# Kernel tuning notes

Hardware: AMD Instinct MI355X
Metric: run time of the kernel (lower is better)

Reference implementation:

```python
import jax, jax.numpy as jnp
import numpy as np

N, E, D_IN, HID, H, L = 20000, 320000, 64, 128, 4, 3
D_HEAD = HID  # PyG TransformerConv: out_channels is the per-head dim
LN_EPS = 1e-5


def setup_inputs() -> dict:
    key = jax.random.key(0)
    ks = jax.random.split(key, 12)
    x = jax.random.normal(ks[0], (N, D_IN), dtype=jnp.float32)
    edge_index = jax.random.randint(ks[1], (2, E), 0, N, dtype=jnp.int64)
    s_in = 1.0 / np.sqrt(D_IN)
    s_h = 1.0 / np.sqrt(HID)
    Win = jax.random.normal(ks[2], (D_IN, HID), dtype=jnp.float32) * s_in
    bin_ = jnp.zeros((HID,), dtype=jnp.float32)
    Wq = jax.random.normal(ks[3], (L, HID, H * D_HEAD), dtype=jnp.float32) * s_h
    Wk = jax.random.normal(ks[4], (L, HID, H * D_HEAD), dtype=jnp.float32) * s_h
    Wv = jax.random.normal(ks[5], (L, HID, H * D_HEAD), dtype=jnp.float32) * s_h
    bq = jnp.zeros((L, H * D_HEAD), dtype=jnp.float32)
    bk = jnp.zeros((L, H * D_HEAD), dtype=jnp.float32)
    bv = jnp.zeros((L, H * D_HEAD), dtype=jnp.float32)
    Wskip = jax.random.normal(ks[6], (L, HID, HID), dtype=jnp.float32) * s_h
    bskip = jnp.zeros((L, HID), dtype=jnp.float32)
    ln_gamma = jnp.ones((L, HID), dtype=jnp.float32)
    ln_beta = jnp.zeros((L, HID), dtype=jnp.float32)
    return dict(x=x, edge_index=edge_index, Win=Win, bin_=bin_, Wq=Wq, bq=bq,
                Wk=Wk, bk=bk, Wv=Wv, bv=bv, Wskip=Wskip, bskip=bskip,
                ln_gamma=ln_gamma, ln_beta=ln_beta)


def _segment_softmax(logits, seg, num_segments):
    # logits: [E, H], seg: [E] destination node ids
    m = jax.ops.segment_max(logits, seg, num_segments=num_segments)  # [N, H]
    ex = jnp.exp(logits - m[seg])
    s = jax.ops.segment_sum(ex, seg, num_segments=num_segments)  # [N, H]
    return ex / (s[seg] + 1e-16)


def _layer_norm(x, gamma, beta):
    mu = jnp.mean(x, axis=-1, keepdims=True)
    var = jnp.mean(jnp.square(x - mu), axis=-1, keepdims=True)
    return (x - mu) * jax.lax.rsqrt(var + LN_EPS) * gamma + beta


def _transformer_conv(h, src, dst, Wq, bq, Wk, bk, Wv, bv, Wskip, bskip):
    q = (h @ Wq + bq).reshape(N, H, D_HEAD)
    k = (h @ Wk + bk).reshape(N, H, D_HEAD)
    v = (h @ Wv + bv).reshape(N, H, D_HEAD)
    scale = 1.0 / np.sqrt(D_HEAD)
    logits = jnp.einsum('ehd,ehd->eh', q[dst], k[src]) * scale  # [E, H]
    alpha = _segment_softmax(logits, dst, N)  # [E, H]
    msg = alpha[:, :, None] * v[src]  # [E, H, D_HEAD]
    out = jax.ops.segment_sum(msg, dst, num_segments=N)  # [N, H, D_HEAD]
    out = out.mean(axis=1)  # concat=False -> mean over heads
    return out + h @ Wskip + bskip  # root_weight skip (lin_skip)


def reference(x, edge_index, Win, bin_, Wq, bq, Wk, bk, Wv, bv, Wskip, bskip, ln_gamma, ln_beta):
    src = edge_index[0]
    dst = edge_index[1]
    h = x @ Win + bin_
    for l in range(L):
        h_new = _transformer_conv(h, src, dst, Wq[l], bq[l], Wk[l], bk[l],
                                  Wv[l], bv[l], Wskip[l], bskip[l])
        h = _layer_norm(h + h_new, ln_gamma[l], ln_beta[l])
    return h
```

## Files before the change

### kernel.cpp

```cpp
#include <hip/hip_runtime.h>
#include <hip/hip_bf16.h>
#include <math.h>

#define NN 20000
#define EE 320000
#define DIN 64
#define HIDC 128
#define NCOLS 1664
#define NL 3

typedef __attribute__((ext_vector_type(8))) short bf16x8;
typedef __attribute__((ext_vector_type(8))) unsigned short u16x8;
typedef __attribute__((ext_vector_type(4))) float f32x4;

__device__ __forceinline__ float bf2f(unsigned short u) {
  union { unsigned i; float f; } v; v.i = ((unsigned)u) << 16; return v.f;
}
__device__ __forceinline__ unsigned short f2bf(float f) {
  __hip_bfloat16 b = __float2bfloat16(f);
  return *(unsigned short*)&b;
}

__device__ __forceinline__ unsigned char f2fp8(float f) {
#if __has_builtin(__builtin_amdgcn_cvt_pk_fp8_f32)
  return (unsigned char)(__builtin_amdgcn_cvt_pk_fp8_f32(f, f, 0, 0) & 0xFF);
#else
  unsigned b = __float_as_uint(f);
  unsigned s = (b >> 24) & 0x80u;
  float a = fabsf(f);
  if (a < 0.015625f) return (unsigned char)s;
  unsigned mag = __float_as_uint(fminf(a, 448.f));
  mag += 0x7FFFFu + ((mag >> 20) & 1u);
  unsigned code = (mag >> 20) - (120u << 3);
  if (code > 0x7Eu) code = 0x7Eu;
  return (unsigned char)(s | code);
#endif
}

__device__ __forceinline__ float fp82f(unsigned b) {
  unsigned x = ((b & 0x80u) << 24) | ((b & 0x7fu) << 20);
  return __uint_as_float(x) * 0x1p+120f;
}

__device__ __forceinline__ void dec8(uint2 u, float* f) {
#if __has_builtin(__builtin_amdgcn_cvt_pk_f32_fp8)
  {
    auto p0 = __builtin_amdgcn_cvt_pk_f32_fp8(u.x, 0);
    auto p1 = __builtin_amdgcn_cvt_pk_f32_fp8(u.x, 1);
    auto p2 = __builtin_amdgcn_cvt_pk_f32_fp8(u.y, 0);
    auto p3 = __builtin_amdgcn_cvt_pk_f32_fp8(u.y, 1);
    f[0] = p0[0]; f[1] = p0[1]; f[2] = p1[0]; f[3] = p1[1];
    f[4] = p2[0]; f[5] = p2[1]; f[6] = p3[0]; f[7] = p3[1];
  }
#else
#pragma unroll
  for (int i = 0; i < 4; i++) f[i] = fp82f((u.x >> (8 * i)) & 0xFFu);
#pragma unroll
  for (int i = 0; i < 4; i++) f[4 + i] = fp82f((u.y >> (8 * i)) & 0xFFu);
#endif
}

__global__ void build_wcatT(const float* __restrict__ Wq, const float* __restrict__ Wk,
                            const float* __restrict__ Wv, const float* __restrict__ Wsk,
                            unsigned short* __restrict__ wT) {
  int idx = blockIdx.x * 256 + threadIdx.x;
  if (idx >= NCOLS * HIDC) return;
  int n = idx >> 7, k = idx & 127;
  float v;
  if (n < 512)       v = Wq[(size_t)k * 512 + n];
  else if (n < 1024) v = Wk[(size_t)k * 512 + (n - 512)];
  else if (n < 1536) v = Wv[(size_t)k * 512 + (n - 1024)];
  else               v = Wsk[(size_t)k * 128 + (n - 1536)];
  wT[idx] = f2bf(v);
}

__global__ void build_winT(const float* __restrict__ Win, unsigned short* __restrict__ winT) {
  int idx = blockIdx.x * 256 + threadIdx.x;
  if (idx >= HIDC * DIN) return;
  int c = idx >> 6, k = idx & 63;
  winT[idx] = f2bf(Win[(size_t)k * HIDC + c]);
}

__global__ void build_bcat(const float* __restrict__ bq, const float* __restrict__ bk,
                           const float* __restrict__ bv, const float* __restrict__ bsk,
                           float* __restrict__ bcat) {
  int m = blockIdx.x * 256 + threadIdx.x;
  if (m >= NCOLS) return;
  float v;
  if (m < 512)       v = bq[m];
  else if (m < 1024) v = bk[m - 512];
  else if (m < 1536) v = bv[m - 1024];
  else               v = bsk[m - 1536];
  bcat[m] = v;
}

__global__ void conv_x(const float* __restrict__ x, unsigned short* __restrict__ xb) {
  int i = blockIdx.x * 256 + threadIdx.x;
  if (i * 4 >= NN * DIN) return;
  float4 v = *(const float4*)(x + (size_t)i * 4);
  ushort4 o = make_ushort4(f2bf(v.x), f2bf(v.y), f2bf(v.z), f2bf(v.w));
  *(ushort4*)(xb + (size_t)i * 4) = o;
}

__global__ void deg_hist(const int* __restrict__ ei, int* __restrict__ deg) {
  int e = blockIdx.x * 256 + threadIdx.x;
  if (e >= EE) return;
  atomicAdd(&deg[ei[EE + e]], 1);
}

__global__ __launch_bounds__(1024) void scan_deg(const int* __restrict__ deg,
                                                 int* __restrict__ rowstart) {
  __shared__ int part[1024];
  int t = threadIdx.x;
  int base = t * 20;
  int local[20];
  int s = 0;
#pragma unroll
  for (int i = 0; i < 20; i++) {
    int idx = base + i;
    int d = (idx < NN) ? deg[idx] : 0;
    local[i] = d;
    s += d;
  }
  part[t] = s;
  __syncthreads();
  for (int d = 1; d < 1024; d <<= 1) {
    int v = (t >= d) ? part[t - d] : 0;
    __syncthreads();
    part[t] += v;
    __syncthreads();
  }
  int run = part[t] - s;
#pragma unroll
  for (int i = 0; i < 20; i++) {
    int idx = base + i;
    if (idx < NN) rowstart[idx] = run;
    run += local[i];
  }
  if (t == 1023) rowstart[NN] = part[1023];
}

__global__ void csr_scatter(const int* __restrict__ ei, const int* __restrict__ rowstart,
                            int* __restrict__ cur, int* __restrict__ csrc) {
  int e = blockIdx.x * 256 + threadIdx.x;
  if (e >= EE) return;
  int src = ei[e], dst = ei[EE + e];
  int pos = atomicAdd(&cur[dst], 1);
  csrc[rowstart[dst] + pos] = src;
}

__device__ __forceinline__ void gl_lds16(const void* g, void* l) {
  __builtin_amdgcn_global_load_lds((const unsigned int*)g, (unsigned int*)l, 16, 0, 0);
}

template <int K>
__device__ __forceinline__ void stage_tile(const unsigned short* gbase,
                                           unsigned char* lbase, int tid) {
  constexpr int CH = K / 8;
  constexpr int ISS = (128 * CH) / 256;
  int wave = tid >> 6;
#pragma unroll
  for (int p = 0; p < ISS; p++) {
    int slot = p * 256 + tid;
    int row = slot / CH, ch = slot % CH;
    const unsigned short* src = gbase + (size_t)row * K + ((ch ^ (row & 7)) * 8);
    unsigned char* ldst = lbase + (size_t)(p * 256 + wave * 64) * 16;
    gl_lds16(src, ldst);
  }
}

template <int K>
__device__ __forceinline__ bf16x8 read_frag(const unsigned char* lbase, int row, int kk, int lk) {
  int ch = (kk * 4 + lk) ^ (row & 7);
  return *(const bf16x8*)(lbase + (size_t)row * (K * 2) + ch * 16);
}

template <int K, int MODE>
__global__ __launch_bounds__(256) void mfma_gemm_t(
    const unsigned short* __restrict__ A, const unsigned short* __restrict__ BT,
    const float* __restrict__ bias, unsigned short* __restrict__ outb,
    unsigned char* __restrict__ outkv, float* __restrict__ outf,
    int nbx, int nwg) {
  constexpr int LDSZ = (512 * K > 34816) ? 512 * K : 34816;
  __shared__ __align__(16) unsigned char LDS[LDSZ];
  const int tid = threadIdx.x;

  int orig = blockIdx.x;
  int q = nwg >> 3, r = nwg & 7;
  int xcd = orig & 7, slot = orig >> 3;
  int wg = (xcd < r ? xcd * (q + 1) : r * (q + 1) + (xcd - r) * q) + slot;
  const int bx = wg % nbx, by = wg / nbx;

  const int lane = tid & 63;
  const int wave = tid >> 6;
  const int lm = lane & 15, lk = lane >> 4;
  const int wm = wave >> 1, wn = wave & 1;
  const int row0 = by * 128, col0 = bx * 128;
  unsigned char* aL = LDS;
  unsigned char* bL = LDS + 128 * K * 2;

  stage_tile<K>(A + (size_t)row0 * K, aL, tid);
  stage_tile<K>(BT + (size_t)col0 * K, bL, tid);
  __syncthreads();

  constexpr int KK = K / 32;
  f32x4 acc[4][4] = {};
  bf16x8 af[4][KK];
#pragma unroll
  for (int mf = 0; mf < 4; mf++)
#pragma unroll
    for (int kk = 0; kk < KK; kk++)
      af[mf][kk] = read_frag<K>(aL, wm * 64 + mf * 16 + lm, kk, lk);

#pragma unroll
  for (int nf = 0; nf < 4; nf++) {
    bf16x8 bf[KK];
#pragma unroll
    for (int kk = 0; kk < KK; kk++)
      bf[kk] = read_frag<K>(bL, wn * 64 + nf * 16 + lm, kk, lk);
#pragma unroll
    for (int mf = 0; mf < 4; mf++)
#pragma unroll
      for (int kk = 0; kk < KK; kk++)
        acc[mf][nf] = __builtin_amdgcn_mfma_f32_16x16x32_bf16(af[mf][kk], bf[kk],
                                                              acc[mf][nf], 0, 0, 0);
  }
  __syncthreads();

  if (MODE == 0 && bx == 12) {
#pragma unroll
    for (int nf = 0; nf < 4; nf++) {
      int c = wn * 64 + nf * 16 + lm;
      float bv = bias[col0 + c];
#pragma unroll
      for (int mf = 0; mf < 4; mf++)
#pragma unroll
        for (int i = 0; i < 4; i++) {
          int rr = row0 + wm * 64 + mf * 16 + lk * 4 + i;
          if (rr < NN) outf[(size_t)rr * HIDC + c] = acc[mf][nf][i] + bv;
        }
    }
  } else if (MODE == 0 && bx >= 4) {
    unsigned char* bb8 = LDS;
#pragma unroll
    for (int nf = 0; nf < 4; nf++) {
      int c = wn * 64 + nf * 16 + lm;
      float bv = bias[col0 + c];
#pragma unroll
      for (int mf = 0; mf < 4; mf++)
#pragma unroll
        for (int i = 0; i < 4; i++) {
          int row = wm * 64 + mf * 16 + lk * 4 + i;
          bb8[row * 144 + c] = f2fp8(acc[mf][nf][i] + bv);
        }
    }
    __syncthreads();
    const int kvcol0 = col0 - 512;
#pragma unroll
    for (int p = 0; p < 4; p++) {
      int idx = p * 256 + tid;
      int row = idx >> 3, cw = idx & 7;
      int gr = row0 + row;
      if (gr < NN) {
        uint4 v = *(const uint4*)(bb8 + row * 144 + cw * 16);
        *(uint4*)(outkv + (size_t)gr * 1024 + kvcol0 + cw * 16) = v;
      }
    }
  } else {
    unsigned short* bb = (unsigned short*)LDS;
#pragma unroll
    for (int nf = 0; nf < 4; nf++) {
      int c = wn * 64 + nf * 16 + lm;
      float bv = bias[col0 + c];
#pragma unroll
      for (int mf = 0; mf < 4; mf++)
#pragma unroll
        for (int i = 0; i < 4; i++) {
          int row = wm * 64 + mf * 16 + lk * 4 + i;
          bb[row * 136 + c] = f2bf(acc[mf][nf][i] + bv);
          if (MODE == 1) {
            int rr = row0 + row;
            if (rr < NN) outf[(size_t)rr * HIDC + c] = acc[mf][nf][i] + bv;
          }
        }
    }
    __syncthreads();
    constexpr int STRIDE = (MODE == 0) ? 512 : HIDC;
#pragma unroll
    for (int p = 0; p < 8; p++) {
      int idx = p * 256 + tid;
      int row = idx >> 4, c = idx & 15;
      int gr = row0 + row;
      if (gr < NN) {
        uint4 v = *(const uint4*)(bb + row * 136 + c * 8);
        *(uint4*)(outb + (size_t)gr * STRIDE + col0 + c * 8) = v;
      }
    }
  }
}

__global__ __launch_bounds__(256) void node_fused(
    const unsigned short* __restrict__ qb, const unsigned char* __restrict__ kv8,
    const float* __restrict__ skipb,
    const float* __restrict__ h, const int* __restrict__ rowstart,
    const int* __restrict__ csrc,
    const float* __restrict__ gamma, const float* __restrict__ beta,
    float* __restrict__ outp, unsigned short* __restrict__ hb_out) {
  int n = blockIdx.x * 4 + (threadIdx.x >> 6);
  if (n >= NN) return;
  int lane = threadIdx.x & 63;
  int hh = lane >> 4, t = lane & 15;
  int j0 = rowstart[n], j1 = rowstart[n + 1];

  u16x8 q8 = *(const u16x8*)(qb + (size_t)n * 512 + hh * 128 + t * 8);
  float qf[8];
#pragma unroll
  for (int i = 0; i < 8; i++) qf[i] = bf2f(q8[i]);

  const unsigned char* kb = kv8 + hh * 128 + t * 8;
  const unsigned char* vb = kv8 + 512 + hh * 128 + t * 8;

  float m = -INFINITY, s = 0.f;
  float acc[8] = {0.f, 0.f, 0.f, 0.f, 0.f, 0.f, 0.f, 0.f};

  int j = j0;
  for (; j + 1 < j1; j += 2) {
    int sA = csrc[j], sB = csrc[j + 1];
    uint2 kA = *(const uint2*)(kb + (size_t)sA * 1024);
    uint2 vA = *(const uint2*)(vb + (size_t)sA * 1024);
    uint2 kB = *(const uint2*)(kb + (size_t)sB * 1024);
    uint2 vB = *(const uint2*)(vb + (size_t)sB * 1024);
    float kfA[8], kfB[8];
    dec8(kA, kfA); dec8(kB, kfB);
    float pA = 0.f, pB = 0.f;
#pragma unroll
    for (int i = 0; i < 8; i++) { pA += qf[i] * kfA[i]; pB += qf[i] * kfB[i]; }
    pA += __shfl_xor(pA, 1); pB += __shfl_xor(pB, 1);
    pA += __shfl_xor(pA, 2); pB += __shfl_xor(pB, 2);
    pA += __shfl_xor(pA, 4); pB += __shfl_xor(pB, 4);
    pA += __shfl_xor(pA, 8); pB += __shfl_xor(pB, 8);
    float lgA = pA * 0.08838834764831845f;
    float lgB = pB * 0.08838834764831845f;
    float vfA[8], vfB[8];
    dec8(vA, vfA); dec8(vB, vfB);
    if (lgA > m) {
      float r = __expf(m - lgA);
      s *= r;
#pragma unroll
      for (int i = 0; i < 8; i++) acc[i] *= r;
      m = lgA;
    }
    float wA = __expf(lgA - m);
    s += wA;
#pragma unroll
    for (int i = 0; i < 8; i++) acc[i] += wA * vfA[i];
    if (lgB > m) {
      float r = __expf(m - lgB);
      s *= r;
#pragma unroll
      for (int i = 0; i < 8; i++) acc[i] *= r;
      m = lgB;
    }
    float wB = __expf(lgB - m);
    s += wB;
#pragma unroll
    for (int i = 0; i < 8; i++) acc[i] += wB * vfB[i];
  }
  if (j < j1) {
    int sA = csrc[j];
    uint2 kA = *(const uint2*)(kb + (size_t)sA * 1024);
    uint2 vA = *(const uint2*)(vb + (size_t)sA * 1024);
    float kfA[8], vfA[8];
    dec8(kA, kfA); dec8(vA, vfA);
    float pA = 0.f;
#pragma unroll
    for (int i = 0; i < 8; i++) pA += qf[i] * kfA[i];
    pA += __shfl_xor(pA, 1);
    pA += __shfl_xor(pA, 2);
    pA += __shfl_xor(pA, 4);
    pA += __shfl_xor(pA, 8);
    float lgA = pA * 0.08838834764831845f;
    if (lgA > m) {
      float r = __expf(m - lgA);
      s *= r;
#pragma unroll
      for (int i = 0; i < 8; i++) acc[i] *= r;
      m = lgA;
    }
    float wA = __expf(lgA - m);
    s += wA;
#pragma unroll
    for (int i = 0; i < 8; i++) acc[i] += wA * vfA[i];
  }

  float rsel = 0.25f / (s + 1e-16f);
#pragma unroll
  for (int i = 0; i < 8; i++) {
    float a = acc[i] * rsel;
    a += __shfl_xor(a, 16);
    a += __shfl_xor(a, 32);
    acc[i] = a;
  }

  size_t hbase = (size_t)n * HIDC;
  float u[8];
  {
    float4 h0 = *(const float4*)(h + hbase + t * 8);
    float4 h1 = *(const float4*)(h + hbase + t * 8 + 4);
    float4 k0 = *(const float4*)(skipb + hbase + t * 8);
    float4 k1 = *(const float4*)(skipb + hbase + t * 8 + 4);
    u[0] = h0.x + acc[0] + k0.x; u[1] = h0.y + acc[1] + k0.y;
    u[2] = h0.z + acc[2] + k0.z; u[3] = h0.w + acc[3] + k0.w;
    u[4] = h1.x + acc[4] + k1.x; u[5] = h1.y + acc[5] + k1.y;
    u[6] = h1.z + acc[6] + k1.z; u[7] = h1.w + acc[7] + k1.w;
  }
  float su = 0.f;
#pragma unroll
  for (int i = 0; i < 8; i++) su += u[i];
#pragma unroll
  for (int d = 1; d < 16; d <<= 1) su += __shfl_xor(su, d);
  float mu = su * (1.f / 128.f);
  float vs = 0.f;
#pragma unroll
  for (int i = 0; i < 8; i++) { u[i] -= mu; vs += u[i] * u[i]; }
#pragma unroll
  for (int d = 1; d < 16; d <<= 1) vs += __shfl_xor(vs, d);
  float inv = rsqrtf(vs * (1.f / 128.f) + 1e-5f);
  if (hh == 0) {
    float4 g0 = *(const float4*)(gamma + t * 8);
    float4 g1 = *(const float4*)(gamma + t * 8 + 4);
    float4 b0 = *(const float4*)(beta + t * 8);
    float4 b1 = *(const float4*)(beta + t * 8 + 4);
    float o[8];
    o[0] = u[0] * inv * g0.x + b0.x; o[1] = u[1] * inv * g0.y + b0.y;
    o[2] = u[2] * inv * g0.z + b0.z; o[3] = u[3] * inv * g0.w + b0.w;
    o[4] = u[4] * inv * g1.x + b1.x; o[5] = u[5] * inv * g1.y + b1.y;
    o[6] = u[6] * inv * g1.z + b1.z; o[7] = u[7] * inv * g1.w + b1.w;
    *(float4*)(outp + hbase + t * 8)     = make_float4(o[0], o[1], o[2], o[3]);
    *(float4*)(outp + hbase + t * 8 + 4) = make_float4(o[4], o[5], o[6], o[7]);
    ushort4 c0 = make_ushort4(f2bf(o[0]), f2bf(o[1]), f2bf(o[2]), f2bf(o[3]));
    ushort4 c1 = make_ushort4(f2bf(o[4]), f2bf(o[5]), f2bf(o[6]), f2bf(o[7]));
    *(ushort4*)(hb_out + hbase + t * 8)     = c0;
    *(ushort4*)(hb_out + hbase + t * 8 + 4) = c1;
  }
}

#define OFF_H      ((size_t)0)
#define OFF_SKIP   ((size_t)2560000)
#define OFF_QB     ((size_t)5120000)
#define OFF_KV8    ((size_t)10240000)
#define OFF_HB     ((size_t)15360000)
#define OFF_XB     ((size_t)16640000)
#define OFF_WT     ((size_t)17280000)
#define OFF_WINT   ((size_t)17386496)
#define OFF_BCAT   ((size_t)17390592)
#define OFF_CSRC   ((size_t)17392256)
#define OFF_ROW    ((size_t)17712256)
#define OFF_DEG    ((size_t)17732260)
#define OFF_CUR    ((size_t)17752260)

extern "C" void kernel_launch(void* const* d_in, const int* in_sizes, int n_in,
                              void* d_out, int out_size, void* d_ws, size_t ws_size,
                              hipStream_t stream) {
  const float* x    = (const float*)d_in[0];
  const int*   ei   = (const int*)d_in[1];
  const float* Win  = (const float*)d_in[2];
  const float* bin_ = (const float*)d_in[3];
  const float* Wq   = (const float*)d_in[4];
  const float* bq   = (const float*)d_in[5];
  const float* Wk   = (const float*)d_in[6];
  const float* bk   = (const float*)d_in[7];
  const float* Wv   = (const float*)d_in[8];
  const float* bv   = (const float*)d_in[9];
  const float* Wsk  = (const float*)d_in[10];
  const float* bsk  = (const float*)d_in[11];
  const float* lng  = (const float*)d_in[12];
  const float* lnb  = (const float*)d_in[13];
  float* out = (float*)d_out;
  float* ws = (float*)d_ws;

  float* h     = ws + OFF_H;
  float* skipb = ws + OFF_SKIP;
  unsigned short* qb   = (unsigned short*)(ws + OFF_QB);
  unsigned char*  kv8  = (unsigned char*)(ws + OFF_KV8);
  unsigned short* hb   = (unsigned short*)(ws + OFF_HB);
  unsigned short* xb   = (unsigned short*)(ws + OFF_XB);
  unsigned short* wT   = (unsigned short*)(ws + OFF_WT);
  unsigned short* winT = (unsigned short*)(ws + OFF_WINT);
  float* bcat  = ws + OFF_BCAT;
  int* csrc     = (int*)(ws + OFF_CSRC);
  int* rowstart = (int*)(ws + OFF_ROW);
  int* deg      = (int*)(ws + OFF_DEG);
  int* cur      = (int*)(ws + OFF_CUR);

  hipMemsetAsync(deg, 0, NN * sizeof(int), stream);
  hipMemsetAsync(cur, 0, NN * sizeof(int), stream);
  deg_hist<<<(EE + 255) / 256, 256, 0, stream>>>(ei, deg);
  scan_deg<<<1, 1024, 0, stream>>>(deg, rowstart);
  csr_scatter<<<(EE + 255) / 256, 256, 0, stream>>>(ei, rowstart, cur, csrc);

  conv_x<<<(NN * DIN / 4 + 255) / 256, 256, 0, stream>>>(x, xb);
  build_winT<<<(HIDC * DIN + 255) / 256, 256, 0, stream>>>(Win, winT);
  {
    const int nby = (NN + 127) / 128;
    mfma_gemm_t<64, 1><<<nby, 256, 0, stream>>>(xb, winT, bin_, hb, kv8, h, 1, nby);
  }

  for (int l = 0; l < NL; ++l) {
    build_wcatT<<<(NCOLS * HIDC + 255) / 256, 256, 0, stream>>>(
        Wq + (size_t)l * HIDC * 512, Wk + (size_t)l * HIDC * 512,
        Wv + (size_t)l * HIDC * 512, Wsk + (size_t)l * HIDC * HIDC, wT);
    build_bcat<<<(NCOLS + 255) / 256, 256, 0, stream>>>(
        bq + (size_t)l * 512, bk + (size_t)l * 512, bv + (size_t)l * 512,
        bsk + (size_t)l * 128, bcat);

    {
      const int nbx = NCOLS / 128;
      const int nby = (NN + 127) / 128;
      const int nwg = nbx * nby;
      mfma_gemm_t<128, 0><<<nwg, 256, 0, stream>>>(hb, wT, bcat, qb, kv8, skipb,
                                                   nbx, nwg);
    }

    float* dst = (l == NL - 1) ? out : h;
    node_fused<<<(NN + 3) / 4, 256, 0, stream>>>(
        qb, kv8, skipb, h, rowstart, csrc,
        lng + (size_t)l * 128, lnb + (size_t)l * 128, dst, hb);
  }
  (void)in_sizes; (void)n_in; (void)out_size; (void)ws_size;
}
```

Baseline: 331.3 us.

## Shrink projection GEMM tiles to 64x64, batch weight prep, unroll edge loop by four

```diff
diff --git a/kernel.cpp b/kernel.cpp
--- a/kernel.cpp
+++ b/kernel.cpp
@@ -60,18 +60,34 @@
 #endif
 }
 
-__global__ void build_wcatT(const float* __restrict__ Wq, const float* __restrict__ Wk,
-                            const float* __restrict__ Wv, const float* __restrict__ Wsk,
-                            unsigned short* __restrict__ wT) {
+__global__ void build_wcatT_all(const float* __restrict__ Wq, const float* __restrict__ Wk,
+                                const float* __restrict__ Wv, const float* __restrict__ Wsk,
+                                unsigned short* __restrict__ wT) {
   int idx = blockIdx.x * 256 + threadIdx.x;
-  if (idx >= NCOLS * HIDC) return;
-  int n = idx >> 7, k = idx & 127;
+  if (idx >= NL * NCOLS * HIDC) return;
+  int l = idx / (NCOLS * HIDC);
+  int rem = idx - l * (NCOLS * HIDC);
+  int n = rem >> 7, k = rem & 127;
   float v;
-  if (n < 512)       v = Wq[(size_t)k * 512 + n];
-  else if (n < 1024) v = Wk[(size_t)k * 512 + (n - 512)];
-  else if (n < 1536) v = Wv[(size_t)k * 512 + (n - 1024)];
-  else               v = Wsk[(size_t)k * 128 + (n - 1536)];
+  if (n < 512)       v = Wq[(size_t)l * HIDC * 512 + (size_t)k * 512 + n];
+  else if (n < 1024) v = Wk[(size_t)l * HIDC * 512 + (size_t)k * 512 + (n - 512)];
+  else if (n < 1536) v = Wv[(size_t)l * HIDC * 512 + (size_t)k * 512 + (n - 1024)];
+  else               v = Wsk[(size_t)l * HIDC * HIDC + (size_t)k * 128 + (n - 1536)];
   wT[idx] = f2bf(v);
+}
+
+__global__ void build_bcat_all(const float* __restrict__ bq, const float* __restrict__ bk,
+                               const float* __restrict__ bv, const float* __restrict__ bsk,
+                               float* __restrict__ bcat) {
+  int idx = blockIdx.x * 256 + threadIdx.x;
+  if (idx >= NL * NCOLS) return;
+  int l = idx / NCOLS, m = idx - l * NCOLS;
+  float v;
+  if (m < 512)       v = bq[l * 512 + m];
+  else if (m < 1024) v = bk[l * 512 + (m - 512)];
+  else if (m < 1536) v = bv[l * 512 + (m - 1024)];
+  else               v = bsk[l * 128 + (m - 1536)];
+  bcat[idx] = v;
 }
 
 __global__ void build_winT(const float* __restrict__ Win, unsigned short* __restrict__ winT) {
@@ -79,19 +95,6 @@
   if (idx >= HIDC * DIN) return;
   int c = idx >> 6, k = idx & 63;
   winT[idx] = f2bf(Win[(size_t)k * HIDC + c]);
-}
-
-__global__ void build_bcat(const float* __restrict__ bq, const float* __restrict__ bk,
-                           const float* __restrict__ bv, const float* __restrict__ bsk,
-                           float* __restrict__ bcat) {
-  int m = blockIdx.x * 256 + threadIdx.x;
-  if (m >= NCOLS) return;
-  float v;
-  if (m < 512)       v = bq[m];
-  else if (m < 1024) v = bk[m - 512];
-  else if (m < 1536) v = bv[m - 1024];
-  else               v = bsk[m - 1536];
-  bcat[m] = v;
 }
 
 __global__ void conv_x(const float* __restrict__ x, unsigned short* __restrict__ xb) {
@@ -175,125 +178,197 @@
   return *(const bf16x8*)(lbase + (size_t)row * (K * 2) + ch * 16);
 }
 
-template <int K, int MODE>
-__global__ __launch_bounds__(256) void mfma_gemm_t(
+__global__ __launch_bounds__(256) void mfma_gemm_in(
     const unsigned short* __restrict__ A, const unsigned short* __restrict__ BT,
     const float* __restrict__ bias, unsigned short* __restrict__ outb,
-    unsigned char* __restrict__ outkv, float* __restrict__ outf,
-    int nbx, int nwg) {
-  constexpr int LDSZ = (512 * K > 34816) ? 512 * K : 34816;
-  __shared__ __align__(16) unsigned char LDS[LDSZ];
+    float* __restrict__ outf) {
+  __shared__ __align__(16) unsigned char LDS[34816];
   const int tid = threadIdx.x;
-
-  int orig = blockIdx.x;
-  int q = nwg >> 3, r = nwg & 7;
-  int xcd = orig & 7, slot = orig >> 3;
-  int wg = (xcd < r ? xcd * (q + 1) : r * (q + 1) + (xcd - r) * q) + slot;
-  const int bx = wg % nbx, by = wg / nbx;
-
-  const int lane = tid & 63;
-  const int wave = tid >> 6;
+  const int lane = tid & 63, wave = tid >> 6;
   const int lm = lane & 15, lk = lane >> 4;
   const int wm = wave >> 1, wn = wave & 1;
-  const int row0 = by * 128, col0 = bx * 128;
+  const int row0 = blockIdx.x * 128, col0 = 0;
   unsigned char* aL = LDS;
-  unsigned char* bL = LDS + 128 * K * 2;
-
-  stage_tile<K>(A + (size_t)row0 * K, aL, tid);
-  stage_tile<K>(BT + (size_t)col0 * K, bL, tid);
+  unsigned char* bL = LDS + 128 * 64 * 2;
+
+  stage_tile<64>(A + (size_t)row0 * 64, aL, tid);
+  stage_tile<64>(BT + (size_t)col0 * 64, bL, tid);
   __syncthreads();
 
-  constexpr int KK = K / 32;
   f32x4 acc[4][4] = {};
-  bf16x8 af[4][KK];
+  bf16x8 af[4][2];
 #pragma unroll
   for (int mf = 0; mf < 4; mf++)
 #pragma unroll
-    for (int kk = 0; kk < KK; kk++)
-      af[mf][kk] = read_frag<K>(aL, wm * 64 + mf * 16 + lm, kk, lk);
-
+    for (int kk = 0; kk < 2; kk++)
+      af[mf][kk] = read_frag<64>(aL, wm * 64 + mf * 16 + lm, kk, lk);
 #pragma unroll
   for (int nf = 0; nf < 4; nf++) {
-    bf16x8 bf[KK];
-#pragma unroll
-    for (int kk = 0; kk < KK; kk++)
-      bf[kk] = read_frag<K>(bL, wn * 64 + nf * 16 + lm, kk, lk);
+    bf16x8 bf[2];
+#pragma unroll
+    for (int kk = 0; kk < 2; kk++)
+      bf[kk] = read_frag<64>(bL, wn * 64 + nf * 16 + lm, kk, lk);
 #pragma unroll
     for (int mf = 0; mf < 4; mf++)
 #pragma unroll
-      for (int kk = 0; kk < KK; kk++)
+      for (int kk = 0; kk < 2; kk++)
         acc[mf][nf] = __builtin_amdgcn_mfma_f32_16x16x32_bf16(af[mf][kk], bf[kk],
                                                               acc[mf][nf], 0, 0, 0);
   }
   __syncthreads();
 
-  if (MODE == 0 && bx == 12) {
-#pragma unroll
-    for (int nf = 0; nf < 4; nf++) {
-      int c = wn * 64 + nf * 16 + lm;
+  unsigned short* bb = (unsigned short*)LDS;
+#pragma unroll
+  for (int nf = 0; nf < 4; nf++) {
+    int c = wn * 64 + nf * 16 + lm;
+    float bv = bias[c];
+#pragma unroll
+    for (int mf = 0; mf < 4; mf++)
+#pragma unroll
+      for (int i = 0; i < 4; i++) {
+        int row = wm * 64 + mf * 16 + lk * 4 + i;
+        float o = acc[mf][nf][i] + bv;
+        bb[row * 136 + c] = f2bf(o);
+        int r = row0 + row;
+        if (r < NN) outf[(size_t)r * HIDC + c] = o;
+      }
+  }
+  __syncthreads();
+#pragma unroll
+  for (int p = 0; p < 8; p++) {
+    int idx = p * 256 + tid;
+    int row = idx >> 4, c = idx & 15;
+    int gr = row0 + row;
+    if (gr < NN) {
+      uint4 v = *(const uint4*)(bb + row * 136 + c * 8);
+      *(uint4*)(outb + (size_t)gr * HIDC + c * 8) = v;
+    }
+  }
+}
+
+__global__ __launch_bounds__(256, 5) void gemm64(
+    const unsigned short* __restrict__ A, const unsigned short* __restrict__ BT,
+    const float* __restrict__ bias, unsigned short* __restrict__ qb,
+    unsigned char* __restrict__ kv8, float* __restrict__ skipb,
+    int nbx, int nwg) {
+  __shared__ __align__(16) unsigned char LDS[32768];
+  const int tid = threadIdx.x;
+  int orig = blockIdx.x;
+  int qq = nwg >> 3, rr8 = nwg & 7;
+  int xcd = orig & 7, slot = orig >> 3;
+  int wg = (xcd < rr8 ? xcd * (qq + 1) : rr8 * (qq + 1) + (xcd - rr8) * qq) + slot;
+  const int bx = wg % nbx, by = wg / nbx;
+
+  const int lane = tid & 63, wave = tid >> 6;
+  const int lm = lane & 15, lk = lane >> 4;
+  const int wm = wave >> 1, wn = wave & 1;
+  const int row0 = by * 64, col0 = bx * 64;
+  unsigned char* aL = LDS;
+  unsigned char* bL = LDS + 16384;
+
+  {
+    const unsigned short* gA = A + (size_t)row0 * 128;
+    const unsigned short* gB = BT + (size_t)col0 * 128;
+#pragma unroll
+    for (int p = 0; p < 4; p++) {
+      int sl = p * 256 + tid;
+      int row = sl >> 4, ch = sl & 15;
+      gl_lds16(gA + (size_t)row * 128 + ((ch ^ (row & 7)) * 8),
+               aL + (size_t)(p * 256 + wave * 64) * 16);
+    }
+#pragma unroll
+    for (int p = 0; p < 4; p++) {
+      int sl = p * 256 + tid;
+      int row = sl >> 4, ch = sl & 15;
+      gl_lds16(gB + (size_t)row * 128 + ((ch ^ (row & 7)) * 8),
+               bL + (size_t)(p * 256 + wave * 64) * 16);
+    }
+  }
+  __syncthreads();
+
+  f32x4 acc[2][2] = {};
+  bf16x8 af[2][4], bf[2][4];
+#pragma unroll
+  for (int mf = 0; mf < 2; mf++)
+#pragma unroll
+    for (int kk = 0; kk < 4; kk++)
+      af[mf][kk] = read_frag<128>(aL, wm * 32 + mf * 16 + lm, kk, lk);
+#pragma unroll
+  for (int nf = 0; nf < 2; nf++)
+#pragma unroll
+    for (int kk = 0; kk < 4; kk++)
+      bf[nf][kk] = read_frag<128>(bL, wn * 32 + nf * 16 + lm, kk, lk);
+#pragma unroll
+  for (int nf = 0; nf < 2; nf++)
+#pragma unroll
+    for (int mf = 0; mf < 2; mf++)
+#pragma unroll
+      for (int kk = 0; kk < 4; kk++)
+        acc[mf][nf] = __builtin_amdgcn_mfma_f32_16x16x32_bf16(af[mf][kk], bf[nf][kk],
+                                                              acc[mf][nf], 0, 0, 0);
+  __syncthreads();
+
+  if (bx >= 24) {
+    const int cbase = col0 - 1536;
+#pragma unroll
+    for (int nf = 0; nf < 2; nf++) {
+      int c = wn * 32 + nf * 16 + lm;
       float bv = bias[col0 + c];
 #pragma unroll
-      for (int mf = 0; mf < 4; mf++)
+      for (int mf = 0; mf < 2; mf++)
 #pragma unroll
         for (int i = 0; i < 4; i++) {
-          int rr = row0 + wm * 64 + mf * 16 + lk * 4 + i;
-          if (rr < NN) outf[(size_t)rr * HIDC + c] = acc[mf][nf][i] + bv;
+          int r = row0 + wm * 32 + mf * 16 + lk * 4 + i;
+          if (r < NN) skipb[(size_t)r * HIDC + cbase + c] = acc[mf][nf][i] + bv;
         }
     }
-  } else if (MODE == 0 && bx >= 4) {
+  } else if (bx >= 8) {
     unsigned char* bb8 = LDS;
 #pragma unroll
-    for (int nf = 0; nf < 4; nf++) {
-      int c = wn * 64 + nf * 16 + lm;
+    for (int nf = 0; nf < 2; nf++) {
+      int c = wn * 32 + nf * 16 + lm;
       float bv = bias[col0 + c];
 #pragma unroll
-      for (int mf = 0; mf < 4; mf++)
+      for (int mf = 0; mf < 2; mf++)
 #pragma unroll
         for (int i = 0; i < 4; i++) {
-          int row = wm * 64 + mf * 16 + lk * 4 + i;
-          bb8[row * 144 + c] = f2fp8(acc[mf][nf][i] + bv);
+          int row = wm * 32 + mf * 16 + lk * 4 + i;
+          bb8[row * 80 + c] = f2fp8(acc[mf][nf][i] + bv);
         }
     }
     __syncthreads();
     const int kvcol0 = col0 - 512;
-#pragma unroll
-    for (int p = 0; p < 4; p++) {
+    {
+      int row = tid >> 2, cw = tid & 3;
+      int gr = row0 + row;
+      if (gr < NN) {
+        uint4 v = *(const uint4*)(bb8 + row * 80 + cw * 16);
+        *(uint4*)(kv8 + (size_t)gr * 1024 + kvcol0 + cw * 16) = v;
+      }
+    }
+  } else {
+    unsigned short* bb = (unsigned short*)LDS;
+#pragma unroll
+    for (int nf = 0; nf < 2; nf++) {
+      int c = wn * 32 + nf * 16 + lm;
+      float bv = bias[col0 + c];
+#pragma unroll
+      for (int mf = 0; mf < 2; mf++)
+#pragma unroll
+        for (int i = 0; i < 4; i++) {
+          int row = wm * 32 + mf * 16 + lk * 4 + i;
+          bb[row * 80 + c] = f2bf(acc[mf][nf][i] + bv);
+        }
+    }
+    __syncthreads();
+#pragma unroll
+    for (int p = 0; p < 2; p++) {
       int idx = p * 256 + tid;
       int row = idx >> 3, cw = idx & 7;
       int gr = row0 + row;
       if (gr < NN) {
-        uint4 v = *(const uint4*)(bb8 + row * 144 + cw * 16);
-        *(uint4*)(outkv + (size_t)gr * 1024 + kvcol0 + cw * 16) = v;
-      }
-    }
-  } else {
-    unsigned short* bb = (unsigned short*)LDS;
-#pragma unroll
-    for (int nf = 0; nf < 4; nf++) {
-      int c = wn * 64 + nf * 16 + lm;
-      float bv = bias[col0 + c];
-#pragma unroll
-      for (int mf = 0; mf < 4; mf++)
-#pragma unroll
-        for (int i = 0; i < 4; i++) {
-          int row = wm * 64 + mf * 16 + lk * 4 + i;
-          bb[row * 136 + c] = f2bf(acc[mf][nf][i] + bv);
-          if (MODE == 1) {
-            int rr = row0 + row;
-            if (rr < NN) outf[(size_t)rr * HIDC + c] = acc[mf][nf][i] + bv;
-          }
-        }
-    }
-    __syncthreads();
-    constexpr int STRIDE = (MODE == 0) ? 512 : HIDC;
-#pragma unroll
-    for (int p = 0; p < 8; p++) {
-      int idx = p * 256 + tid;
-      int row = idx >> 4, c = idx & 15;
-      int gr = row0 + row;
-      if (gr < NN) {
-        uint4 v = *(const uint4*)(bb + row * 136 + c * 8);
-        *(uint4*)(outb + (size_t)gr * STRIDE + col0 + c * 8) = v;
+        uint4 v = *(const uint4*)(bb + row * 80 + cw * 8);
+        *(uint4*)(qb + (size_t)gr * 512 + col0 + cw * 8) = v;
       }
     }
   }
@@ -324,49 +399,49 @@
   float acc[8] = {0.f, 0.f, 0.f, 0.f, 0.f, 0.f, 0.f, 0.f};
 
   int j = j0;
-  for (; j + 1 < j1; j += 2) {
-    int sA = csrc[j], sB = csrc[j + 1];
-    uint2 kA = *(const uint2*)(kb + (size_t)sA * 1024);
-    uint2 vA = *(const uint2*)(vb + (size_t)sA * 1024);
-    uint2 kB = *(const uint2*)(kb + (size_t)sB * 1024);
-    uint2 vB = *(const uint2*)(vb + (size_t)sB * 1024);
-    float kfA[8], kfB[8];
-    dec8(kA, kfA); dec8(kB, kfB);
-    float pA = 0.f, pB = 0.f;
-#pragma unroll
-    for (int i = 0; i < 8; i++) { pA += qf[i] * kfA[i]; pB += qf[i] * kfB[i]; }
-    pA += __shfl_xor(pA, 1); pB += __shfl_xor(pB, 1);
-    pA += __shfl_xor(pA, 2); pB += __shfl_xor(pB, 2);
-    pA += __shfl_xor(pA, 4); pB += __shfl_xor(pB, 4);
-    pA += __shfl_xor(pA, 8); pB += __shfl_xor(pB, 8);
-    float lgA = pA * 0.08838834764831845f;
-    float lgB = pB * 0.08838834764831845f;
-    float vfA[8], vfB[8];
-    dec8(vA, vfA); dec8(vB, vfB);
-    if (lgA > m) {
-      float r = __expf(m - lgA);
-      s *= r;
-#pragma unroll
-      for (int i = 0; i < 8; i++) acc[i] *= r;
-      m = lgA;
-    }
-    float wA = __expf(lgA - m);
-    s += wA;
-#pragma unroll
-    for (int i = 0; i < 8; i++) acc[i] += wA * vfA[i];
-    if (lgB > m) {
-      float r = __expf(m - lgB);
-      s *= r;
-#pragma unroll
-      for (int i = 0; i < 8; i++) acc[i] *= r;
-      m = lgB;
-    }
-    float wB = __expf(lgB - m);
-    s += wB;
-#pragma unroll
-    for (int i = 0; i < 8; i++) acc[i] += wB * vfB[i];
-  }
-  if (j < j1) {
+  for (; j + 3 < j1; j += 4) {
+    int s4[4];
+#pragma unroll
+    for (int e = 0; e < 4; e++) s4[e] = csrc[j + e];
+    uint2 kk4[4], vv4[4];
+#pragma unroll
+    for (int e = 0; e < 4; e++) {
+      kk4[e] = *(const uint2*)(kb + (size_t)s4[e] * 1024);
+      vv4[e] = *(const uint2*)(vb + (size_t)s4[e] * 1024);
+    }
+    float lg4[4];
+#pragma unroll
+    for (int e = 0; e < 4; e++) {
+      float kf[8];
+      dec8(kk4[e], kf);
+      float p = 0.f;
+#pragma unroll
+      for (int i = 0; i < 8; i++) p += qf[i] * kf[i];
+      p += __shfl_xor(p, 1);
+      p += __shfl_xor(p, 2);
+      p += __shfl_xor(p, 4);
+      p += __shfl_xor(p, 8);
+      lg4[e] = p * 0.08838834764831845f;
+    }
+    float mx = fmaxf(fmaxf(lg4[0], lg4[1]), fmaxf(lg4[2], lg4[3]));
+    if (mx > m) {
+      float rr = __expf(m - mx);
+      s *= rr;
+#pragma unroll
+      for (int i = 0; i < 8; i++) acc[i] *= rr;
+      m = mx;
+    }
+#pragma unroll
+    for (int e = 0; e < 4; e++) {
+      float w = __expf(lg4[e] - m);
+      s += w;
+      float vf[8];
+      dec8(vv4[e], vf);
+#pragma unroll
+      for (int i = 0; i < 8; i++) acc[i] += w * vf[i];
+    }
+  }
+  for (; j < j1; ++j) {
     int sA = csrc[j];
     uint2 kA = *(const uint2*)(kb + (size_t)sA * 1024);
     uint2 vA = *(const uint2*)(vb + (size_t)sA * 1024);
@@ -381,10 +456,10 @@
     pA += __shfl_xor(pA, 8);
     float lgA = pA * 0.08838834764831845f;
     if (lgA > m) {
-      float r = __expf(m - lgA);
-      s *= r;
-#pragma unroll
-      for (int i = 0; i < 8; i++) acc[i] *= r;
+      float rr = __expf(m - lgA);
+      s *= rr;
+#pragma unroll
+      for (int i = 0; i < 8; i++) acc[i] *= rr;
       m = lgA;
     }
     float wA = __expf(lgA - m);
@@ -452,12 +527,12 @@
 #define OFF_HB     ((size_t)15360000)
 #define OFF_XB     ((size_t)16640000)
 #define OFF_WT     ((size_t)17280000)
-#define OFF_WINT   ((size_t)17386496)
-#define OFF_BCAT   ((size_t)17390592)
-#define OFF_CSRC   ((size_t)17392256)
-#define OFF_ROW    ((size_t)17712256)
-#define OFF_DEG    ((size_t)17732260)
-#define OFF_CUR    ((size_t)17752260)
+#define OFF_WINT   ((size_t)17599488)
+#define OFF_BCAT   ((size_t)17603584)
+#define OFF_CSRC   ((size_t)17608576)
+#define OFF_ROW    ((size_t)17928576)
+#define OFF_DEG    ((size_t)17948580)
+#define OFF_CUR    ((size_t)17968580)
 
 extern "C" void kernel_launch(void* const* d_in, const int* in_sizes, int n_in,
                               void* d_out, int out_size, void* d_ws, size_t ws_size,
@@ -501,26 +576,20 @@
 
   conv_x<<<(NN * DIN / 4 + 255) / 256, 256, 0, stream>>>(x, xb);
   build_winT<<<(HIDC * DIN + 255) / 256, 256, 0, stream>>>(Win, winT);
-  {
-    const int nby = (NN + 127) / 128;
-    mfma_gemm_t<64, 1><<<nby, 256, 0, stream>>>(xb, winT, bin_, hb, kv8, h, 1, nby);
-  }
+  build_wcatT_all<<<(NL * NCOLS * HIDC + 255) / 256, 256, 0, stream>>>(
+      Wq, Wk, Wv, Wsk, wT);
+  build_bcat_all<<<(NL * NCOLS + 255) / 256, 256, 0, stream>>>(bq, bk, bv, bsk, bcat);
+
+  mfma_gemm_in<<<(NN + 127) / 128, 256, 0, stream>>>(xb, winT, bin_, hb, h);
+
+  const int nbx = NCOLS / 64;
+  const int nby = (NN + 63) / 64;
+  const int nwg = nbx * nby;
 
   for (int l = 0; l < NL; ++l) {
-    build_wcatT<<<(NCOLS * HIDC + 255) / 256, 256, 0, stream>>>(
-        Wq + (size_t)l * HIDC * 512, Wk + (size_t)l * HIDC * 512,
-        Wv + (size_t)l * HIDC * 512, Wsk + (size_t)l * HIDC * HIDC, wT);
-    build_bcat<<<(NCOLS + 255) / 256, 256, 0, stream>>>(
-        bq + (size_t)l * 512, bk + (size_t)l * 512, bv + (size_t)l * 512,
-        bsk + (size_t)l * 128, bcat);
-
-    {
-      const int nbx = NCOLS / 128;
-      const int nby = (NN + 127) / 128;
-      const int nwg = nbx * nby;
-      mfma_gemm_t<128, 0><<<nwg, 256, 0, stream>>>(hb, wT, bcat, qb, kv8, skipb,
-                                                   nbx, nwg);
-    }
+    gemm64<<<nwg, 256, 0, stream>>>(hb, wT + (size_t)l * NCOLS * HIDC,
+                                    bcat + (size_t)l * NCOLS, qb, kv8, skipb,
+                                    nbx, nwg);
 
     float* dst = (l == NL - 1) ? out : h;
     node_fused<<<(NN + 3) / 4, 256, 0, stream>>>(
```

Measured after the change: 312.9 us. -5.5%, faster.
